# Kernel tuning notes

Hardware: AMD Instinct MI355X
Metric: run time of the kernel (lower is better)

The kernel has to match this reference:

```python
import jax, jax.numpy as jnp
import numpy as np

B, S, H = 4, 2048, 576
NH, NKV, HD = 9, 3, 64
GROUPS = NH // NKV
ROPE_THETA = 100000.0
MAX_POS = 8192


def _rope_tables():
    inv_freq = 1.0 / (ROPE_THETA ** (jnp.arange(0, HD, 2, dtype=jnp.float32) / HD))
    t = jnp.arange(MAX_POS, dtype=jnp.float32)
    freqs = jnp.outer(t, inv_freq)              # [MAX_POS, HD//2]
    emb = jnp.concatenate([freqs, freqs], axis=-1)  # [MAX_POS, HD]
    return jnp.cos(emb), jnp.sin(emb)


def _rotate_half(x):
    x1, x2 = x[..., : HD // 2], x[..., HD // 2 :]
    return jnp.concatenate([-x2, x1], axis=-1)


def setup_inputs() -> dict:
    key = jax.random.key(0)
    k1, k2, k3, k4, k5 = jax.random.split(key, 5)
    hidden_states = jax.random.normal(k1, (B, S, H), dtype=jnp.float32)
    # causal additive mask [B,1,S,S]: 0 where allowed, large negative above diagonal
    causal = jnp.triu(jnp.ones((S, S), dtype=bool), k=1)
    attention_mask = jnp.where(causal, jnp.float32(-1e9), jnp.float32(0.0))[None, None]
    attention_mask = jnp.broadcast_to(attention_mask, (B, 1, S, S))
    position_ids = jnp.broadcast_to(jnp.arange(S, dtype=jnp.int32)[None, :], (B, S))
    scale = 1.0 / np.sqrt(H)
    Wq = jax.random.normal(k2, (NH * HD, H), dtype=jnp.float32) * scale
    Wk = jax.random.normal(k3, (NKV * HD, H), dtype=jnp.float32) * scale
    Wv = jax.random.normal(k4, (NKV * HD, H), dtype=jnp.float32) * scale
    Wo = jax.random.normal(k5, (H, NH * HD), dtype=jnp.float32) * scale
    return {"hidden_states": hidden_states, "attention_mask": attention_mask,
            "position_ids": position_ids, "Wq": Wq, "Wk": Wk, "Wv": Wv, "Wo": Wo}


def reference(hidden_states, attention_mask, position_ids, Wq, Wk, Wv, Wo):
    bsz, q_len, _ = hidden_states.shape
    cos_cached, sin_cached = _rope_tables()
    # projections (nn.Linear: x @ W.T), reshape to [B, heads, S, HD]
    q = (hidden_states @ Wq.T).reshape(bsz, q_len, NH, HD).transpose(0, 2, 1, 3)
    k = (hidden_states @ Wk.T).reshape(bsz, q_len, NKV, HD).transpose(0, 2, 1, 3)
    v = (hidden_states @ Wv.T).reshape(bsz, q_len, NKV, HD).transpose(0, 2, 1, 3)
    # RoPE: gather cos/sin per position, broadcast over heads
    cos = cos_cached[position_ids][:, None]  # [B,1,S,HD]
    sin = sin_cached[position_ids][:, None]
    q = q * cos + _rotate_half(q) * sin
    k = k * cos + _rotate_half(k) * sin
    # GQA: repeat_interleave kv heads
    k = jnp.repeat(k, GROUPS, axis=1)  # [B,NH,S,HD]
    v = jnp.repeat(v, GROUPS, axis=1)
    scores = jnp.einsum('bhqd,bhkd->bhqk', q, k) / np.sqrt(HD)
    scores = scores + attention_mask
    probs = jax.nn.softmax(scores.astype(jnp.float32), axis=-1).astype(q.dtype)
    attn = jnp.einsum('bhqk,bhkd->bhqd', probs, v)
    attn = attn.transpose(0, 2, 1, 3).reshape(bsz, q_len, NH * HD)
    return attn @ Wo.T
```

## Files before the change

kernel.cpp:

```cpp
#include <hip/hip_runtime.h>
#include <hip/hip_bf16.h>
#include <math.h>

#define Bsz 4
#define Slen 2048
#define Hdim 576
#define NH 9
#define NKV 3
#define HD 64

typedef __bf16 bf16_t;
typedef __bf16 bf16x8 __attribute__((ext_vector_type(8)));
typedef float f32x4 __attribute__((ext_vector_type(4)));
typedef float f32x16 __attribute__((ext_vector_type(16)));
typedef unsigned int u32;
typedef unsigned int u32x4 __attribute__((ext_vector_type(4)));

static __device__ __forceinline__ bf16x8 load_cvt8(const float* __restrict__ src){
  float4 f0 = *reinterpret_cast<const float4*>(src);
  float4 f1 = *reinterpret_cast<const float4*>(src + 4);
  bf16x8 v;
  v[0]=(bf16_t)f0.x; v[1]=(bf16_t)f0.y; v[2]=(bf16_t)f0.z; v[3]=(bf16_t)f0.w;
  v[4]=(bf16_t)f1.x; v[5]=(bf16_t)f1.y; v[6]=(bf16_t)f1.z; v[7]=(bf16_t)f1.w;
  return v;
}

static __device__ __forceinline__ void gload16(const bf16_t* g, bf16_t* l){
  __builtin_amdgcn_global_load_lds((const __attribute__((address_space(1))) void*)g,
                                   (__attribute__((address_space(3))) void*)l, 16, 0, 0);
}

__global__ void rope_table_kernel(float* __restrict__ cost, float* __restrict__ sint){
  int i = blockIdx.x * blockDim.x + threadIdx.x;
  if (i >= Slen * 32) return;
  int j = i & 31;
  int p = i >> 5;
  double invf = pow(100000.0, -(double)j / 32.0);
  double ang = (double)p * invf;
  cost[i] = (float)cos(ang);
  sint[i] = (float)sin(ang);
}

__global__ void precast_kernel(const float* __restrict__ X,
                               const float* __restrict__ Wq,
                               const float* __restrict__ Wk,
                               const float* __restrict__ Wv,
                               const float* __restrict__ Wo,
                               bf16_t* __restrict__ Xb,
                               bf16_t* __restrict__ Wb,
                               bf16_t* __restrict__ Wob)
{
  const int NX  = 8192 * 576 / 8;
  const int NWq = 576 * 576 / 8;
  const int NWk = 192 * 576 / 8;
  int i = blockIdx.x * blockDim.x + threadIdx.x;
  const int total = NX + NWq + 2 * NWk + NWq;
  if (i >= total) return;
  const float* src; bf16_t* dst; int off;
  if (i < NX)                    { src = X;  dst = Xb;            off = i; }
  else if (i < NX + NWq)         { src = Wq; dst = Wb;            off = i - NX; }
  else if (i < NX + NWq + NWk)   { src = Wk; dst = Wb + 331776;   off = i - NX - NWq; }
  else if (i < NX + NWq + 2*NWk) { src = Wv; dst = Wb + 442368;   off = i - NX - NWq - NWk; }
  else                           { src = Wo; dst = Wob;           off = i - NX - NWq - 2*NWk; }
  *reinterpret_cast<bf16x8*>(dst + (size_t)off * 8) = load_cvt8(src + (size_t)off * 8);
}

__launch_bounds__(256)
__global__ void qkv_gemm_kernel(const bf16_t* __restrict__ Xb,
                                const bf16_t* __restrict__ Wb,
                                bf16_t* __restrict__ qbuf,
                                bf16_t* __restrict__ kbuf,
                                bf16_t* __restrict__ vtbuf)
{
  __shared__ bf16_t Ald[2][128 * 64];
  __shared__ bf16_t Bld[2][64 * 64];
  const int t = threadIdx.x, l = t & 63, w = t >> 6;
  const int wm = w >> 1, wn = w & 1;
  const int lane16 = l & 15, grp = l >> 4;
  const int m0 = blockIdx.x * 128;
  const int nt = blockIdx.y;
  const int nrow0 = nt * 64;

  const int sr = l >> 3;
  const int sc = ((l & 7) ^ sr) * 8;

  f32x4 acc[4][2];
  #pragma unroll
  for (int mi = 0; mi < 4; ++mi)
    #pragma unroll
    for (int ni = 0; ni < 2; ++ni)
      acc[mi][ni] = (f32x4){0.f, 0.f, 0.f, 0.f};

  auto STAGE = [&](int kt, int buf){
    const int k0 = kt * 64;
    #pragma unroll
    for (int u = 0; u < 4; ++u)
      gload16(Xb + (size_t)(m0 + w * 32 + u * 8 + sr) * Hdim + k0 + sc,
              &Ald[buf][(w * 32 + u * 8) * 64]);
    #pragma unroll
    for (int u = 0; u < 2; ++u)
      gload16(Wb + (size_t)(nrow0 + w * 16 + u * 8 + sr) * Hdim + k0 + sc,
              &Bld[buf][(w * 16 + u * 8) * 64]);
  };

  STAGE(0, 0);
  asm volatile("s_waitcnt vmcnt(0)" ::: "memory");
  __syncthreads();

  const int sl7 = lane16 & 7;
  for (int kt = 0; kt < 9; ++kt){
    const int buf = kt & 1;
    if (kt + 1 < 9) STAGE(kt + 1, buf ^ 1);
    #pragma unroll
    for (int ks = 0; ks < 2; ++ks){
      bf16x8 a[4], bb[2];
      #pragma unroll
      for (int mi = 0; mi < 4; ++mi){
        int row = wm * 64 + mi * 16 + lane16;
        a[mi] = *reinterpret_cast<const bf16x8*>(&Ald[buf][row * 64 + (((ks * 4 + grp) ^ sl7) * 8)]);
      }
      #pragma unroll
      for (int ni = 0; ni < 2; ++ni){
        int row = wn * 32 + ni * 16 + lane16;
        bb[ni] = *reinterpret_cast<const bf16x8*>(&Bld[buf][row * 64 + (((ks * 4 + grp) ^ sl7) * 8)]);
      }
      #pragma unroll
      for (int mi = 0; mi < 4; ++mi)
        #pragma unroll
        for (int ni = 0; ni < 2; ++ni)
          acc[mi][ni] = __builtin_amdgcn_mfma_f32_16x16x32_bf16(a[mi], bb[ni], acc[mi][ni], 0, 0, 0);
    }
    if (kt + 1 < 9){
      asm volatile("s_waitcnt vmcnt(0)" ::: "memory");
      __syncthreads();
    }
  }

  #pragma unroll
  for (int mi = 0; mi < 4; ++mi){
    #pragma unroll
    for (int ni = 0; ni < 2; ++ni){
      #pragma unroll
      for (int j = 0; j < 4; ++j){
        int m = m0 + wm * 64 + mi * 16 + grp * 4 + j;
        int dl = wn * 32 + ni * 16 + lane16;
        int b = m >> 11;
        int s = m & 2047;
        bf16_t v = (bf16_t)acc[mi][ni][j];
        if (nt < 9)
          qbuf[(((size_t)b * NH + nt) * Slen + s) * HD + dl] = v;
        else if (nt < 12)
          kbuf[(((size_t)b * NKV + (nt - 9)) * Slen + s) * HD + dl] = v;
        else
          vtbuf[(((size_t)b * NKV + (nt - 12)) * HD + dl) * Slen + s] = v;
      }
    }
  }
}

__global__ void rope_apply_all(bf16_t* __restrict__ qkbuf, const int* __restrict__ pos_ids,
                               const float* __restrict__ cost, const float* __restrict__ sint,
                               float qscale)
{
  int idx = blockIdx.x * blockDim.x + threadIdx.x;
  const int qrows = Bsz * NH * Slen;
  const int total = qrows + Bsz * NKV * Slen;
  if (idx >= total) return;
  const bool isq = idx < qrows;
  int s = idx & (Slen - 1);
  int b = isq ? idx / (NH * Slen) : (idx - qrows) / (NKV * Slen);
  float scale = isq ? qscale : 1.0f;
  bf16_t* row = qkbuf + (size_t)idx * HD;
  int pos = pos_ids[b * Slen + s];
  const float* cp = cost + (size_t)pos * 32;
  const float* sp = sint + (size_t)pos * 32;
  float x[64];
  #pragma unroll
  for (int v = 0; v < 8; ++v){
    bf16x8 t8 = *reinterpret_cast<const bf16x8*>(row + v * 8);
    #pragma unroll
    for (int i = 0; i < 8; ++i) x[v * 8 + i] = (float)t8[i];
  }
  bf16_t o[64];
  #pragma unroll
  for (int j = 0; j < 32; ++j){
    float c = cp[j], sn = sp[j];
    o[j]      = (bf16_t)((x[j] * c - x[j + 32] * sn) * scale);
    o[j + 32] = (bf16_t)((x[j + 32] * c + x[j] * sn) * scale);
  }
  #pragma unroll
  for (int v = 0; v < 8; ++v)
    *reinterpret_cast<bf16x8*>(row + v * 8) = *reinterpret_cast<bf16x8*>(o + v * 8);
}

__launch_bounds__(128)
__global__ void flash_attn_kernel(const bf16_t* __restrict__ qbuf,
                                  const bf16_t* __restrict__ kbuf,
                                  const bf16_t* __restrict__ vtbuf,
                                  bf16_t* __restrict__ attn_out,
                                  u32* __restrict__ part_O,
                                  float* __restrict__ part_ml)
{
  __shared__ bf16_t Kld[2][64 * 64];
  __shared__ bf16_t Vld[2][64 * 64];
  const int t = threadIdx.x, l = t & 63, w = t >> 6;
  const int l32 = l & 31, hi = l >> 5;

  const int flat = blockIdx.x;
  const int v = flat / 36;
  const int bh = flat % 36;
  int qt, t0, t1, seg;
  if (v < 16){ qt = 16 + v; t0 = 0; t1 = 16; seg = 0; }
  else {
    int i = (v - 16) >> 1;
    if (((v - 16) & 1) == 0){ qt = 15 - i; t0 = 0; t1 = qt + 1; seg = -1; }
    else                    { qt = 31 - i; t0 = 16; t1 = qt + 1; seg = 1; }
  }
  const int b = bh / NH, h = bh % NH, kvh = h / (NH / NKV);

  const bf16_t* qp = qbuf + ((size_t)b * NH + h) * Slen * HD;
  const bf16_t* kp = kbuf + ((size_t)b * NKV + kvh) * Slen * HD;
  const bf16_t* vp = vtbuf + ((size_t)b * NKV + kvh) * HD * Slen;

  const int q0 = qt * 64 + w * 32;
  bf16x8 aq[4];
  #pragma unroll
  for (int ds = 0; ds < 4; ++ds)
    aq[ds] = *reinterpret_cast<const bf16x8*>(qp + (size_t)(q0 + l32) * HD + ds * 16 + hi * 8);

  f32x16 acco[2];
  #pragma unroll
  for (int db = 0; db < 2; ++db)
    #pragma unroll
    for (int r = 0; r < 16; ++r) acco[db][r] = 0.f;
  float mrun = -1e30f, lrun = 0.f;

  const int sr = l >> 3;
  const int sc = ((l & 7) ^ sr) * 8;

  auto STAGE = [&](int kt, int buf){
    const int k0 = kt * 64;
    #pragma unroll
    for (int u = 0; u < 4; ++u){
      int r = (w * 4 + u) * 8 + sr;
      gload16(kp + (size_t)(k0 + r) * HD + sc, &Kld[buf][(w * 4 + u) * 512]);
      gload16(vp + (size_t)r * Slen + k0 + sc, &Vld[buf][(w * 4 + u) * 512]);
    }
  };

  int cur = 0;
  STAGE(t0, 0);
  asm volatile("s_waitcnt vmcnt(0)" ::: "memory");
  __syncthreads();

  for (int kb = t0; kb < t1; ++kb){
    if (kb + 1 < t1) STAGE(kb + 1, cur ^ 1);

    f32x16 sacc[2];
    #pragma unroll
    for (int kb2 = 0; kb2 < 2; ++kb2)
      #pragma unroll
      for (int r = 0; r < 16; ++r) sacc[kb2][r] = 0.f;

    __builtin_amdgcn_s_setprio(1);
    #pragma unroll
    for (int ds = 0; ds < 4; ++ds){
      #pragma unroll
      for (int kb2 = 0; kb2 < 2; ++kb2){
        int row = kb2 * 32 + l32;
        bf16x8 ak = *reinterpret_cast<const bf16x8*>(
            &Kld[cur][row * 64 + (((ds * 2 + hi) ^ (row & 7)) * 8)]);
        sacc[kb2] = __builtin_amdgcn_mfma_f32_32x32x16_bf16(ak, aq[ds], sacc[kb2], 0, 0, 0);
      }
    }
    __builtin_amdgcn_s_setprio(0);

    if (kb == qt){
      const int q_wt = w * 32 + l32;
      #pragma unroll
      for (int kb2 = 0; kb2 < 2; ++kb2)
        #pragma unroll
        for (int r = 0; r < 16; ++r){
          int k_wt = kb2 * 32 + (r & 3) + 8 * (r >> 2) + 4 * hi;
          if (k_wt > q_wt) sacc[kb2][r] = -1e30f;
        }
    }

    float tmax;
    {
      float m0_ = fmaxf(sacc[0][0], sacc[0][1]);
      #pragma unroll
      for (int r = 2; r < 16; ++r) m0_ = fmaxf(m0_, sacc[0][r]);
      float m1_ = fmaxf(sacc[1][0], sacc[1][1]);
      #pragma unroll
      for (int r = 2; r < 16; ++r) m1_ = fmaxf(m1_, sacc[1][r]);
      tmax = fmaxf(m0_, m1_);
    }
    tmax = fmaxf(tmax, __shfl_xor(tmax, 32, 64));

    if (__ballot(tmax - mrun > 8.f)){
      float mnew = fmaxf(mrun, tmax);
      float sf = __builtin_amdgcn_exp2f(mrun - mnew);
      lrun *= sf;
      #pragma unroll
      for (int db = 0; db < 2; ++db)
        #pragma unroll
        for (int r = 0; r < 16; ++r) acco[db][r] *= sf;
      mrun = mnew;
    }

    float rs0 = 0.f, rs1 = 0.f;
    #pragma unroll
    for (int kb2 = 0; kb2 < 2; ++kb2){
      #pragma unroll
      for (int r = 0; r < 16; ++r){
        float p = __builtin_amdgcn_exp2f(sacc[kb2][r] - mrun);
        sacc[kb2][r] = p;
        if (kb2) rs1 += p; else rs0 += p;
      }
    }
    float rsum = rs0 + rs1;
    rsum += __shfl_xor(rsum, 32, 64);
    lrun += rsum;

    u32x4 pa[4];
    #pragma unroll
    for (int kb2 = 0; kb2 < 2; ++kb2){
      u32 wv[8];
      #pragma unroll
      for (int j = 0; j < 8; ++j){
        float lo = sacc[kb2][2 * j], hp = sacc[kb2][2 * j + 1];
        asm("v_cvt_pk_bf16_f32 %0, %1, %2" : "=v"(wv[j]) : "v"(lo), "v"(hp));
      }
      asm volatile("v_permlane32_swap_b32 %0, %1" : "+v"(wv[0]), "+v"(wv[2]));
      asm volatile("v_permlane32_swap_b32 %0, %1" : "+v"(wv[1]), "+v"(wv[3]));
      asm volatile("v_permlane32_swap_b32 %0, %1" : "+v"(wv[4]), "+v"(wv[6]));
      asm volatile("v_permlane32_swap_b32 %0, %1" : "+v"(wv[5]), "+v"(wv[7]));
      pa[2 * kb2]     = (u32x4){wv[0], wv[1], wv[2], wv[3]};
      pa[2 * kb2 + 1] = (u32x4){wv[4], wv[5], wv[6], wv[7]};
    }

    __builtin_amdgcn_s_setprio(1);
    #pragma unroll
    for (int ks = 0; ks < 4; ++ks){
      #pragma unroll
      for (int db = 0; db < 2; ++db){
        int row = db * 32 + l32;
        bf16x8 av = *reinterpret_cast<const bf16x8*>(
            &Vld[cur][row * 64 + (((ks * 2 + hi) ^ (row & 7)) * 8)]);
        acco[db] = __builtin_amdgcn_mfma_f32_32x32x16_bf16(
            av, __builtin_bit_cast(bf16x8, pa[ks]), acco[db], 0, 0, 0);
      }
    }
    __builtin_amdgcn_s_setprio(0);

    asm volatile("s_waitcnt vmcnt(0)" ::: "memory");
    __syncthreads();
    cur ^= 1;
  }

  if (seg < 0){
    const float linv = 1.0f / lrun;
    const int srow = q0 + l32;
    bf16_t* orow = attn_out + ((size_t)b * Slen + srow) * (NH * HD) + h * HD;
    #pragma unroll
    for (int db = 0; db < 2; ++db){
      #pragma unroll
      for (int j = 0; j < 8; ++j){
        int r = 2 * j;
        int d = db * 32 + (r & 3) + 8 * (r >> 2) + 4 * hi;
        u32 pw;
        float lo = acco[db][r] * linv, hp = acco[db][r + 1] * linv;
        asm("v_cvt_pk_bf16_f32 %0, %1, %2" : "=v"(pw) : "v"(lo), "v"(hp));
        *reinterpret_cast<u32*>(orow + d) = pw;
      }
    }
  } else {
    const int slot = (bh * 16 + (qt - 16)) * 2 + seg;
    u32* po = part_O + ((size_t)slot * 2 + w) * 1024;
    float* pml = part_ml + ((size_t)slot * 2 + w) * 64;
    #pragma unroll
    for (int db = 0; db < 2; ++db){
      #pragma unroll
      for (int j = 0; j < 8; ++j){
        int r = 2 * j;
        int d = db * 32 + (r & 3) + 8 * (r >> 2) + 4 * hi;
        u32 pw;
        float lo = acco[db][r], hp = acco[db][r + 1];
        asm("v_cvt_pk_bf16_f32 %0, %1, %2" : "=v"(pw) : "v"(lo), "v"(hp));
        po[(d >> 1) * 32 + l32] = pw;
      }
    }
    if (hi == 0){ pml[l32] = mrun; pml[32 + l32] = lrun; }
  }
}

__launch_bounds__(128)
__global__ void combine_kernel(const u32* __restrict__ part_O,
                               const float* __restrict__ part_ml,
                               bf16_t* __restrict__ attn_out)
{
  const int idx = blockIdx.x;
  const int bh = idx % 36, qtm = idx / 36;
  const int qt = 16 + qtm;
  const int b = bh / NH, h = bh % NH;
  const int t = threadIdx.x;
  const int q = t & 31, wg = (t >> 5) & 1, half = t >> 6;
  const int slot0 = (bh * 16 + qtm) * 2;

  const float* pml0 = part_ml + ((size_t)(slot0 + 0) * 2 + wg) * 64;
  const float* pml1 = part_ml + ((size_t)(slot0 + 1) * 2 + wg) * 64;
  float m1 = pml0[q], l1 = pml0[32 + q];
  float m2 = pml1[q], l2 = pml1[32 + q];
  float m = fmaxf(m1, m2);
  float a1 = __builtin_amdgcn_exp2f(m1 - m);
  float a2 = __builtin_amdgcn_exp2f(m2 - m);
  float linv = 1.0f / (l1 * a1 + l2 * a2);
  a1 *= linv; a2 *= linv;

  const u32* po0 = part_O + ((size_t)(slot0 + 0) * 2 + wg) * 1024;
  const u32* po1 = part_O + ((size_t)(slot0 + 1) * 2 + wg) * 1024;
  const int s = qt * 64 + wg * 32 + q;
  bf16_t* orow = attn_out + ((size_t)b * Slen + s) * (NH * HD) + h * HD;

  #pragma unroll
  for (int u = 0; u < 16; ++u){
    int dp = half * 16 + u;
    u32 v1 = po0[dp * 32 + q], v2 = po1[dp * 32 + q];
    float lo = a1 * __builtin_bit_cast(float, v1 << 16)
             + a2 * __builtin_bit_cast(float, v2 << 16);
    float hv = a1 * __builtin_bit_cast(float, v1 & 0xffff0000u)
             + a2 * __builtin_bit_cast(float, v2 & 0xffff0000u);
    u32 pw;
    asm("v_cvt_pk_bf16_f32 %0, %1, %2" : "=v"(pw) : "v"(lo), "v"(hv));
    *reinterpret_cast<u32*>(orow + 2 * dp) = pw;
  }
}

__launch_bounds__(256)
__global__ void out_gemm_kernel(const bf16_t* __restrict__ A,
                                const bf16_t* __restrict__ Wob,
                                float* __restrict__ out)
{
  __shared__ bf16_t Ald[2][128 * 64];
  __shared__ bf16_t Bld[2][64 * 64];
  const int t = threadIdx.x, l = t & 63, w = t >> 6;
  const int wm = w >> 1, wn = w & 1;
  const int lane16 = l & 15, grp = l >> 4;
  const int m0 = blockIdx.x * 128;
  const int nt = blockIdx.y;
  const int nrow0 = nt * 64;

  const int sr = l >> 3;
  const int sc = ((l & 7) ^ sr) * 8;

  f32x4 acc[4][2];
  #pragma unroll
  for (int mi = 0; mi < 4; ++mi)
    #pragma unroll
    for (int ni = 0; ni < 2; ++ni)
      acc[mi][ni] = (f32x4){0.f, 0.f, 0.f, 0.f};

  auto STAGE = [&](int kt, int buf){
    const int k0 = kt * 64;
    #pragma unroll
    for (int u = 0; u < 4; ++u)
      gload16(A + (size_t)(m0 + w * 32 + u * 8 + sr) * Hdim + k0 + sc,
              &Ald[buf][(w * 32 + u * 8) * 64]);
    #pragma unroll
    for (int u = 0; u < 2; ++u)
      gload16(Wob + (size_t)(nrow0 + w * 16 + u * 8 + sr) * Hdim + k0 + sc,
              &Bld[buf][(w * 16 + u * 8) * 64]);
  };

  STAGE(0, 0);
  asm volatile("s_waitcnt vmcnt(0)" ::: "memory");
  __syncthreads();

  const int sl7 = lane16 & 7;
  for (int kt = 0; kt < 9; ++kt){
    const int buf = kt & 1;
    if (kt + 1 < 9) STAGE(kt + 1, buf ^ 1);
    #pragma unroll
    for (int ks = 0; ks < 2; ++ks){
      bf16x8 a[4], bb[2];
      #pragma unroll
      for (int mi = 0; mi < 4; ++mi){
        int row = wm * 64 + mi * 16 + lane16;
        a[mi] = *reinterpret_cast<const bf16x8*>(&Ald[buf][row * 64 + (((ks * 4 + grp) ^ sl7) * 8)]);
      }
      #pragma unroll
      for (int ni = 0; ni < 2; ++ni){
        int row = wn * 32 + ni * 16 + lane16;
        bb[ni] = *reinterpret_cast<const bf16x8*>(&Bld[buf][row * 64 + (((ks * 4 + grp) ^ sl7) * 8)]);
      }
      #pragma unroll
      for (int mi = 0; mi < 4; ++mi)
        #pragma unroll
        for (int ni = 0; ni < 2; ++ni)
          acc[mi][ni] = __builtin_amdgcn_mfma_f32_16x16x32_bf16(a[mi], bb[ni], acc[mi][ni], 0, 0, 0);
    }
    if (kt + 1 < 9){
      asm volatile("s_waitcnt vmcnt(0)" ::: "memory");
      __syncthreads();
    }
  }

  #pragma unroll
  for (int mi = 0; mi < 4; ++mi){
    #pragma unroll
    for (int ni = 0; ni < 2; ++ni){
      #pragma unroll
      for (int j = 0; j < 4; ++j){
        int m = m0 + wm * 64 + mi * 16 + grp * 4 + j;
        int n = nrow0 + wn * 32 + ni * 16 + lane16;
        out[(size_t)m * Hdim + n] = acc[mi][ni][j];
      }
    }
  }
}

extern "C" void kernel_launch(void* const* d_in, const int* in_sizes, int n_in,
                              void* d_out, int out_size, void* d_ws, size_t ws_size,
                              hipStream_t stream) {
  const float* X   = (const float*)d_in[0];
  const int* pos   = (const int*)d_in[2];
  const float* Wq  = (const float*)d_in[3];
  const float* Wk  = (const float*)d_in[4];
  const float* Wv  = (const float*)d_in[5];
  const float* Wo  = (const float*)d_in[6];
  float* out = (float*)d_out;

  char* ws = (char*)d_ws;
  float* cost = (float*)ws;
  float* sint = (float*)(ws + 262144);
  bf16_t* qb  = (bf16_t*)(ws + 524288);
  bf16_t* kb  = qb + (size_t)Bsz * NH * Slen * HD;
  bf16_t* vt  = kb + (size_t)Bsz * NKV * Slen * HD;
  bf16_t* Xb  = vt + (size_t)Bsz * NKV * Slen * HD;
  bf16_t* ab  = Xb;
  bf16_t* Wb  = Xb + (size_t)8192 * 576;
  bf16_t* Wob = Wb + (size_t)960 * 576;
  u32*  part_O  = (u32*)(Wob + (size_t)576 * 576);
  float* part_ml = (float*)(part_O + (size_t)1152 * 2 * 1024);

  const float QSCALE = 0.125f * 1.44269504088896f;

  rope_table_kernel<<<dim3((Slen * 32 + 255) / 256), dim3(256), 0, stream>>>(cost, sint);
  precast_kernel<<<dim3(2736), dim3(256), 0, stream>>>(X, Wq, Wk, Wv, Wo, Xb, Wb, Wob);
  qkv_gemm_kernel<<<dim3(64, 15), dim3(256), 0, stream>>>(Xb, Wb, qb, kb, vt);
  rope_apply_all<<<dim3((Bsz * (NH + NKV) * Slen + 255) / 256), dim3(256), 0, stream>>>(qb, pos, cost, sint, QSCALE);
  flash_attn_kernel<<<dim3(1728), dim3(128), 0, stream>>>(qb, kb, vt, ab, part_O, part_ml);
  combine_kernel<<<dim3(576), dim3(128), 0, stream>>>(part_O, part_ml, ab);
  out_gemm_kernel<<<dim3(64, 9), dim3(256), 0, stream>>>(ab, Wob, out);
}
```

Baseline: 119.4 us.

## Shrink key tile to 32 and skip fully-masked per-warp tiles

Changes the flash-attention inner loop from 64-key tiles to 32-key tiles, with per-warp diagonal tracking so each 32-row warp skips key tiles entirely above its causal diagonal. The aim is to cut wasted MFMA and softmax work on masked blocks near the diagonal and to halve LDS staging per iteration. In exchange the loop runs twice as many iterations, each with its own barrier and smaller MFMA batches, so synchronisation overhead and latency exposure per key grow.

```diff
diff --git a/kernel.cpp b/kernel.cpp
--- a/kernel.cpp
+++ b/kernel.cpp
@@ -201,8 +201,8 @@
                                   u32* __restrict__ part_O,
                                   float* __restrict__ part_ml)
 {
-  __shared__ bf16_t Kld[2][64 * 64];
-  __shared__ bf16_t Vld[2][64 * 64];
+  __shared__ bf16_t Kld[2][32 * 64];
+  __shared__ bf16_t Vld[2][64 * 32];
   const int t = threadIdx.x, l = t & 63, w = t >> 6;
   const int l32 = l & 31, hi = l >> 5;
 
@@ -210,11 +210,11 @@
   const int v = flat / 36;
   const int bh = flat % 36;
   int qt, t0, t1, seg;
-  if (v < 16){ qt = 16 + v; t0 = 0; t1 = 16; seg = 0; }
+  if (v < 16){ qt = 16 + v; t0 = 0; t1 = 32; seg = 0; }
   else {
     int i = (v - 16) >> 1;
-    if (((v - 16) & 1) == 0){ qt = 15 - i; t0 = 0; t1 = qt + 1; seg = -1; }
-    else                    { qt = 31 - i; t0 = 16; t1 = qt + 1; seg = 1; }
+    if (((v - 16) & 1) == 0){ qt = 15 - i; t0 = 0; t1 = 2 * qt + 2; seg = -1; }
+    else                    { qt = 31 - i; t0 = 32; t1 = 2 * qt + 2; seg = 1; }
   }
   const int b = bh / NH, h = bh % NH, kvh = h / (NH / NKV);
 
@@ -235,16 +235,18 @@
     for (int r = 0; r < 16; ++r) acco[db][r] = 0.f;
   float mrun = -1e30f, lrun = 0.f;
 
-  const int sr = l >> 3;
-  const int sc = ((l & 7) ^ sr) * 8;
+  const int krow = l >> 3;
+  const int ksc  = ((l & 7) ^ krow) * 8;
+  const int vrow = l >> 2;
+  const int vsc  = ((l & 3) ^ (vrow & 3)) * 8;
 
   auto STAGE = [&](int kt, int buf){
-    const int k0 = kt * 64;
-    #pragma unroll
-    for (int u = 0; u < 4; ++u){
-      int r = (w * 4 + u) * 8 + sr;
-      gload16(kp + (size_t)(k0 + r) * HD + sc, &Kld[buf][(w * 4 + u) * 512]);
-      gload16(vp + (size_t)r * Slen + k0 + sc, &Vld[buf][(w * 4 + u) * 512]);
+    const int k0 = kt * 32;
+    #pragma unroll
+    for (int u = 0; u < 2; ++u){
+      int ub = w * 2 + u;
+      gload16(kp + (size_t)(k0 + ub * 8 + krow) * HD + ksc, &Kld[buf][ub * 512]);
+      gload16(vp + (size_t)(ub * 16 + vrow) * Slen + k0 + vsc, &Vld[buf][ub * 512]);
     }
   };
 
@@ -253,106 +255,83 @@
   asm volatile("s_waitcnt vmcnt(0)" ::: "memory");
   __syncthreads();
 
+  const int dt = 2 * qt + w;
   for (int kb = t0; kb < t1; ++kb){
     if (kb + 1 < t1) STAGE(kb + 1, cur ^ 1);
 
-    f32x16 sacc[2];
-    #pragma unroll
-    for (int kb2 = 0; kb2 < 2; ++kb2)
-      #pragma unroll
-      for (int r = 0; r < 16; ++r) sacc[kb2][r] = 0.f;
-
-    __builtin_amdgcn_s_setprio(1);
-    #pragma unroll
-    for (int ds = 0; ds < 4; ++ds){
-      #pragma unroll
-      for (int kb2 = 0; kb2 < 2; ++kb2){
-        int row = kb2 * 32 + l32;
+    if (kb <= dt){
+      f32x16 sacc;
+      #pragma unroll
+      for (int r = 0; r < 16; ++r) sacc[r] = 0.f;
+      __builtin_amdgcn_s_setprio(1);
+      #pragma unroll
+      for (int ds = 0; ds < 4; ++ds){
         bf16x8 ak = *reinterpret_cast<const bf16x8*>(
-            &Kld[cur][row * 64 + (((ds * 2 + hi) ^ (row & 7)) * 8)]);
-        sacc[kb2] = __builtin_amdgcn_mfma_f32_32x32x16_bf16(ak, aq[ds], sacc[kb2], 0, 0, 0);
-      }
-    }
-    __builtin_amdgcn_s_setprio(0);
-
-    if (kb == qt){
-      const int q_wt = w * 32 + l32;
-      #pragma unroll
-      for (int kb2 = 0; kb2 < 2; ++kb2)
+            &Kld[cur][l32 * 64 + (((ds * 2 + hi) ^ (l32 & 7)) * 8)]);
+        sacc = __builtin_amdgcn_mfma_f32_32x32x16_bf16(ak, aq[ds], sacc, 0, 0, 0);
+      }
+      __builtin_amdgcn_s_setprio(0);
+
+      if (kb == dt){
         #pragma unroll
         for (int r = 0; r < 16; ++r){
-          int k_wt = kb2 * 32 + (r & 3) + 8 * (r >> 2) + 4 * hi;
-          if (k_wt > q_wt) sacc[kb2][r] = -1e30f;
+          int crow = (r & 3) + 8 * (r >> 2) + 4 * hi;
+          if (crow > l32) sacc[r] = -1e30f;
         }
-    }
-
-    float tmax;
-    {
-      float m0_ = fmaxf(sacc[0][0], sacc[0][1]);
-      #pragma unroll
-      for (int r = 2; r < 16; ++r) m0_ = fmaxf(m0_, sacc[0][r]);
-      float m1_ = fmaxf(sacc[1][0], sacc[1][1]);
-      #pragma unroll
-      for (int r = 2; r < 16; ++r) m1_ = fmaxf(m1_, sacc[1][r]);
-      tmax = fmaxf(m0_, m1_);
-    }
-    tmax = fmaxf(tmax, __shfl_xor(tmax, 32, 64));
-
-    if (__ballot(tmax - mrun > 8.f)){
-      float mnew = fmaxf(mrun, tmax);
-      float sf = __builtin_amdgcn_exp2f(mrun - mnew);
-      lrun *= sf;
-      #pragma unroll
-      for (int db = 0; db < 2; ++db)
+      }
+
+      float tmax = fmaxf(sacc[0], sacc[1]);
+      #pragma unroll
+      for (int r = 2; r < 16; ++r) tmax = fmaxf(tmax, sacc[r]);
+      tmax = fmaxf(tmax, __shfl_xor(tmax, 32, 64));
+
+      if (__ballot(tmax - mrun > 8.f)){
+        float mnew = fmaxf(mrun, tmax);
+        float sf = __builtin_amdgcn_exp2f(mrun - mnew);
+        lrun *= sf;
         #pragma unroll
-        for (int r = 0; r < 16; ++r) acco[db][r] *= sf;
-      mrun = mnew;
-    }
-
-    float rs0 = 0.f, rs1 = 0.f;
-    #pragma unroll
-    for (int kb2 = 0; kb2 < 2; ++kb2){
+        for (int db = 0; db < 2; ++db)
+          #pragma unroll
+          for (int r = 0; r < 16; ++r) acco[db][r] *= sf;
+        mrun = mnew;
+      }
+
+      float rsum = 0.f;
       #pragma unroll
       for (int r = 0; r < 16; ++r){
-        float p = __builtin_amdgcn_exp2f(sacc[kb2][r] - mrun);
-        sacc[kb2][r] = p;
-        if (kb2) rs1 += p; else rs0 += p;
-      }
-    }
-    float rsum = rs0 + rs1;
-    rsum += __shfl_xor(rsum, 32, 64);
-    lrun += rsum;
-
-    u32x4 pa[4];
-    #pragma unroll
-    for (int kb2 = 0; kb2 < 2; ++kb2){
+        float pv = __builtin_amdgcn_exp2f(sacc[r] - mrun);
+        sacc[r] = pv;
+        rsum += pv;
+      }
+      rsum += __shfl_xor(rsum, 32, 64);
+      lrun += rsum;
+
       u32 wv[8];
       #pragma unroll
       for (int j = 0; j < 8; ++j){
-        float lo = sacc[kb2][2 * j], hp = sacc[kb2][2 * j + 1];
+        float lo = sacc[2 * j], hp = sacc[2 * j + 1];
         asm("v_cvt_pk_bf16_f32 %0, %1, %2" : "=v"(wv[j]) : "v"(lo), "v"(hp));
       }
       asm volatile("v_permlane32_swap_b32 %0, %1" : "+v"(wv[0]), "+v"(wv[2]));
       asm volatile("v_permlane32_swap_b32 %0, %1" : "+v"(wv[1]), "+v"(wv[3]));
       asm volatile("v_permlane32_swap_b32 %0, %1" : "+v"(wv[4]), "+v"(wv[6]));
       asm volatile("v_permlane32_swap_b32 %0, %1" : "+v"(wv[5]), "+v"(wv[7]));
-      pa[2 * kb2]     = (u32x4){wv[0], wv[1], wv[2], wv[3]};
-      pa[2 * kb2 + 1] = (u32x4){wv[4], wv[5], wv[6], wv[7]};
-    }
-
-    __builtin_amdgcn_s_setprio(1);
-    #pragma unroll
-    for (int ks = 0; ks < 4; ++ks){
-      #pragma unroll
-      for (int db = 0; db < 2; ++db){
-        int row = db * 32 + l32;
-        bf16x8 av = *reinterpret_cast<const bf16x8*>(
-            &Vld[cur][row * 64 + (((ks * 2 + hi) ^ (row & 7)) * 8)]);
-        acco[db] = __builtin_amdgcn_mfma_f32_32x32x16_bf16(
-            av, __builtin_bit_cast(bf16x8, pa[ks]), acco[db], 0, 0, 0);
-      }
-    }
-    __builtin_amdgcn_s_setprio(0);
+      u32x4 pa0 = (u32x4){wv[0], wv[1], wv[2], wv[3]};
+      u32x4 pa1 = (u32x4){wv[4], wv[5], wv[6], wv[7]};
+
+      __builtin_amdgcn_s_setprio(1);
+      #pragma unroll
+      for (int ks = 0; ks < 2; ++ks){
+        #pragma unroll
+        for (int db = 0; db < 2; ++db){
+          bf16x8 av = *reinterpret_cast<const bf16x8*>(
+              &Vld[cur][(db * 32 + l32) * 32 + (((ks * 2 + hi) ^ (l32 & 3)) * 8)]);
+          acco[db] = __builtin_amdgcn_mfma_f32_32x32x16_bf16(
+              av, __builtin_bit_cast(bf16x8, ks ? pa1 : pa0), acco[db], 0, 0, 0);
+        }
+      }
+      __builtin_amdgcn_s_setprio(0);
+    }
 
     asm volatile("s_waitcnt vmcnt(0)" ::: "memory");
     __syncthreads();
```

Result: no change. 118.9 us (-0.4%).
